# Performance work log

Measured on AMD Instinct MI355X. Metric: run time of the kernel, lower is better.

The kernel has to match this reference:

```python
import jax, jax.numpy as jnp
import numpy as np

H = 128  # hidden_size hard-coded in the torch module


def _lin(key, fan_in, shape):
    b = 1.0 / np.sqrt(fan_in)
    return jax.random.uniform(key, shape, minval=-b, maxval=b, dtype=jnp.float32)


def _gru_step(x, wih, bih, bhh):
    # torch GRU, single time step, h0 = 0; gate order (r, z, n)
    g = x @ wih.T + bih
    xr, xz, xn = jnp.split(g, 3, axis=-1)
    br, bz, bn = jnp.split(bhh, 3)
    r = jax.nn.sigmoid(xr + br)
    z = jax.nn.sigmoid(xz + bz)
    n = jnp.tanh(xn + r * bn)
    return (1.0 - z) * n  # h' = (1-z)*n + z*0


def _forward(x_node, x_edge, nt_w1, nt_b1, nt_w2, nt_b2, et_w, et_b,
             ngru_wih, ngru_bih, ngru_bhh, egru_wih, egru_bih, egru_bhh,
             natt_w, natt_b, eatt_w, eatt_b,
             lr_w1, lr_b1, lr_w2, lr_b2, cr_w1, cr_b1, cr_w2, cr_b2,
             mr_w1, mr_b1, mr_w2, mr_b2, pairs):
    B, N, _ = x_node.shape
    node_f = jax.nn.relu(x_node @ nt_w1 + nt_b1) @ nt_w2 + nt_b2      # [B,N,H]
    edge_f = x_edge @ et_w + et_b                                      # [B,N,N,H]
    nh = eh = None
    for _ in range(2):  # num_time_steps; GRU inputs are NOT updated in the original loop
        nh = _gru_step(node_f, ngru_wih, ngru_bih, ngru_bhh)           # [B,N,H]
        eh = _gru_step(edge_f, egru_wih, egru_bih, egru_bhh)           # [B,N,N,H]
        # --- node message pooling: attention over column index j ---
        n_col = jnp.broadcast_to(nh[:, :, None, :], eh.shape)          # aug[b,i,j] = nh[b,i]
        logits = (jnp.concatenate([n_col, eh], -1) @ natt_w)[..., 0] + natt_b[0]
        w = jax.nn.softmax(logits, axis=-1)                            # [B,N,N]
        nh = jnp.einsum('bijk,bij->bik', eh, w)                        # pooled node states
        # --- edge message pooling: 2-way attention over (row, col) node states ---
        n_row = jnp.broadcast_to(nh[:, None, :, :], eh.shape)          # [b,i,j] = nh[b,j]
        n_col = jnp.broadcast_to(nh[:, :, None, :], eh.shape)          # [b,i,j] = nh[b,i]
        l_row = (jnp.concatenate([n_row, eh], -1) @ eatt_w)[..., 0] + eatt_b[0]
        l_col = (jnp.concatenate([n_col, eh], -1) @ eatt_w)[..., 0] + eatt_b[0]
        w2 = jax.nn.softmax(jnp.stack([l_row, l_col], -1), axis=-1)    # [B,N,N,2]
        eh = w2[..., 0:1] * n_row + w2[..., 1:2] * n_col               # einsum('bijl,bijkl->bijk')
    # --- classifier inputs (aggregator = elementwise mean) ---
    i0, i1 = pairs[..., 0], pairs[..., 1]                              # [B,P]
    emb0 = jnp.take_along_axis(nh, i0[..., None], axis=1)              # [B,P,H]
    emb1 = jnp.take_along_axis(nh, i1[..., None], axis=1)
    bix = jnp.arange(B)[:, None]
    e01 = eh[bix, i0, i1]                                              # [B,P,H]
    e10 = eh[bix, i1, i0]
    ci = jnp.concatenate([(emb0 + emb1) * 0.5, (e01 + e10) * 0.5], -1)  # [B,P,2H]

    def head(w1, b1, wo, bo):
        return jax.nn.relu(ci @ w1 + b1) @ wo + bo

    lr = head(lr_w1, lr_b1, lr_w2, lr_b2)
    cr = head(cr_w1, cr_b1, cr_w2, cr_b2)
    mr = head(mr_w1, mr_b1, mr_w2, mr_b2)
    return jnp.concatenate([lr, cr, mr], axis=-1)                      # [B,P,6+5+3]


def setup_inputs() -> dict:
    B, N, P = 16, 64, 128
    NF, EF = 1024, 512
    CH = 512  # classifier hidden
    ks = list(jax.random.split(jax.random.key(0), 40))
    k = iter(ks)
    inp = {}
    inp['concatenated_node_features'] = jax.random.normal(next(k), (B, N, NF), dtype=jnp.float32)
    inp['interaction_feature'] = jax.random.normal(next(k), (B, N, N, EF), dtype=jnp.float32)
    inp['nt_w1'] = _lin(next(k), NF, (NF, 512)); inp['nt_b1'] = _lin(next(k), NF, (512,))
    inp['nt_w2'] = _lin(next(k), 512, (512, H)); inp['nt_b2'] = _lin(next(k), 512, (H,))
    inp['et_w'] = _lin(next(k), EF, (EF, H)); inp['et_b'] = _lin(next(k), EF, (H,))
    inp['ngru_wih'] = _lin(next(k), H, (3 * H, H))
    inp['ngru_bih'] = _lin(next(k), H, (3 * H,)); inp['ngru_bhh'] = _lin(next(k), H, (3 * H,))
    inp['egru_wih'] = _lin(next(k), H, (3 * H, H))
    inp['egru_bih'] = _lin(next(k), H, (3 * H,)); inp['egru_bhh'] = _lin(next(k), H, (3 * H,))
    inp['natt_w'] = _lin(next(k), 2 * H, (2 * H, 1)); inp['natt_b'] = _lin(next(k), 2 * H, (1,))
    inp['eatt_w'] = _lin(next(k), 2 * H, (2 * H, 1)); inp['eatt_b'] = _lin(next(k), 2 * H, (1,))
    for name, od in (('lr', 6), ('cr', 5), ('mr', 3)):
        inp[name + '_w1'] = _lin(next(k), 2 * H, (2 * H, CH))
        inp[name + '_b1'] = _lin(next(k), 2 * H, (CH,))
        inp[name + '_w2'] = _lin(next(k), CH, (CH, od))
        inp[name + '_b2'] = _lin(next(k), CH, (od,))
    inp['object_pairs'] = jax.random.randint(next(k), (B, P, 2), 0, N, dtype=jnp.int64 if jax.config.jax_enable_x64 else jnp.int32)
    inp['num_relation'] = jax.random.randint(next(k), (B,), 0, P, dtype=jnp.int64 if jax.config.jax_enable_x64 else jnp.int32)
    return inp


def reference(concatenated_node_features, interaction_feature,
              nt_w1, nt_b1, nt_w2, nt_b2, et_w, et_b,
              ngru_wih, ngru_bih, ngru_bhh, egru_wih, egru_bih, egru_bhh,
              natt_w, natt_b, eatt_w, eatt_b,
              lr_w1, lr_b1, lr_w2, lr_b2, cr_w1, cr_b1, cr_w2, cr_b2,
              mr_w1, mr_b1, mr_w2, mr_b2, object_pairs, num_relation):
    # num_relation is read but unused in the original make_classifier_inputs loop
    return _forward(concatenated_node_features, interaction_feature,
                    nt_w1, nt_b1, nt_w2, nt_b2, et_w, et_b,
                    ngru_wih, ngru_bih, ngru_bhh, egru_wih, egru_bih, egru_bhh,
                    natt_w, natt_b, eatt_w, eatt_b,
                    lr_w1, lr_b1, lr_w2, lr_b2, cr_w1, cr_b1, cr_w2, cr_b2,
                    mr_w1, mr_b1, mr_w2, mr_b2, object_pairs)
```

## Files before the change

kernel.cpp:

```cpp
#include <hip/hip_runtime.h>
#include <math.h>
#include <stdint.h>


typedef __attribute__((ext_vector_type(8))) short short8;
typedef __attribute__((ext_vector_type(4))) float f32x4;

#define DEVINL __device__ __forceinline__

DEVINL float sigmoidf_(float x) { return 1.0f / (1.0f + __expf(-x)); }
DEVINL float tanhf_(float x) {
    float e = __expf(2.0f * x);
    return (e - 1.0f) / (e + 1.0f);
}
DEVINL short bf16_rne(float f) {
    uint32_t u = __float_as_uint(f);
    u += 0x7FFFu + ((u >> 16) & 1u);
    return (short)(u >> 16);
}
DEVINL float bf16_to_f(short s) {
    return __uint_as_float(((uint32_t)(uint16_t)s) << 16);
}
DEVINL void cvt_hilo8(const float av[8], short8* h8, short8* l8) {
    union { uint32_t u[4]; short8 s; } H, L;
#pragma unroll
    for (int i = 0; i < 4; ++i) {
        float a0 = av[2 * i], a1 = av[2 * i + 1];
        uint32_t ph;
        asm("v_cvt_pk_bf16_f32 %0, %1, %2" : "=v"(ph) : "v"(a0), "v"(a1));
        float h0 = __uint_as_float(ph << 16);
        float h1 = __uint_as_float(ph & 0xFFFF0000u);
        uint32_t pl;
        asm("v_cvt_pk_bf16_f32 %0, %1, %2" : "=v"(pl) : "v"(a0 - h0), "v"(a1 - h1));
        H.u[i] = ph;
        L.u[i] = pl;
    }
    *h8 = H.s;
    *l8 = L.s;
}
DEVINL void gload_lds16(const void* g, void* l) {
    __builtin_amdgcn_global_load_lds(
        (const __attribute__((address_space(1))) void*)(uintptr_t)g,
        (__attribute__((address_space(3))) void*)(uint32_t)(uintptr_t)l,
        16, 0, 0);
}
DEVINL void ldsbar() {
    asm volatile("s_waitcnt lgkmcnt(0)\n\ts_barrier" ::: "memory");
    __builtin_amdgcn_sched_barrier(0);
}

__global__ __launch_bounds__(256) void prep_all(
    const float* __restrict__ et_w, const float* __restrict__ wih,
    const float* __restrict__ w1a, const float* __restrict__ w1b,
    const float* __restrict__ w1c,
    short* __restrict__ Bf1, short* __restrict__ Bf2,
    short* __restrict__ Wf1_hi, short* __restrict__ Wf1_lo)
{
    const int bid = blockIdx.x, t = threadIdx.x;
    if (bid < 256) {
        int idx = bid * 256 + t;
        int k = idx >> 7, n = idx & 127;
        float v = et_w[(size_t)k * 128 + n];
        short hi = bf16_rne(v);
        int kt = k >> 5, ct = n >> 4;
        int lane = (((k >> 3) & 3) << 4) | (n & 15);
        int j = k & 7;
        size_t s0 = (((size_t)kt * 8 + ct) * 64 + lane) * 8 + j;
        Bf1[s0] = hi;
    } else if (bid < 448) {
        int idx = (bid - 256) * 256 + t;
        int n = idx >> 7, k = idx & 127;
        float v = wih[(size_t)n * 128 + k];
        short hi = bf16_rne(v);
        int kt = k >> 5, ct = n >> 4;
        int lane = (((k >> 3) & 3) << 4) | (n & 15);
        int j = k & 7;
        size_t s0 = (((size_t)kt * 24 + ct) * 64 + lane) * 8 + j;
        Bf2[s0] = hi;
    } else {
        int idx = (bid - 448) * 256 + t;
        int h = idx >> 17;
        int r = idx & 131071;
        int k = r >> 9, c = r & 511;
        const float* w1 = (h == 0) ? w1a : (h == 1) ? w1b : w1c;
        float v = w1[(size_t)k * 512 + c];
        short hi = bf16_rne(v), lo = bf16_rne(v - bf16_to_f(hi));
        int kt = k >> 5, ct = c >> 4;
        int lane = (((k >> 3) & 3) << 4) | (c & 15);
        int j = k & 7;
        size_t fidx = ((((size_t)h * 8 + kt) * 32 + ct) * 64 + lane) * 8 + j;
        Wf1_hi[fidx] = hi;
        Wf1_lo[fidx] = lo;
    }
}

#define PH1_ITER(KT, BH0, BH1, NBH0, NBH1,                                    \
                 PCV0, PCV1, PLD0, PLD1, RBUF, WBUF)                          \
    {                                                                         \
        if ((KT) < 15) {                                                      \
            const short* bkt = Bf1 + (size_t)((KT) + 1) * 4096;               \
            NBH0 = *(const short8*)(bkt + ct0 * 512 + ln8);                   \
            NBH1 = *(const short8*)(bkt + ct1 * 512 + ln8);                   \
            float av[8] = {PCV0.x, PCV0.y, PCV0.z, PCV0.w,                    \
                           PCV1.x, PCV1.y, PCV1.z, PCV1.w};                   \
            short8 h8, l8;                                                    \
            cvt_hilo8(av, &h8, &l8);                                          \
            *(short8*)(smem + (WBUF) + aslotb) = h8;                          \
            *(short8*)(smem + (WBUF) + 4096 + aslotb) = l8;                   \
        }                                                                     \
        if ((KT) < 14) {                                                      \
            PLD0 = *(const float4*)(aptr + (size_t)((KT) + 2) * 32);          \
            PLD1 = *(const float4*)(aptr + (size_t)((KT) + 2) * 32 + 4);      \
        }                                                                     \
        {                                                                     \
            const char* Ah_c = smem + (RBUF);                                 \
            short8 Ahf[4], Alf[4];                                            \
            _Pragma("unroll") for (int rt = 0; rt < 4; ++rt) {                \
                Ahf[rt] = *(const short8*)(Ah_c + (rt * 64 + lane) * 16);     \
                Alf[rt] = *(const short8*)(Ah_c + 4096 + (rt * 64 + lane) * 16); \
            }                                                                 \
            _Pragma("unroll") for (int rt = 0; rt < 4; ++rt) {                \
                acc1[rt][0] = __builtin_amdgcn_mfma_f32_16x16x32_bf16(Ahf[rt], BH0, acc1[rt][0], 0, 0, 0); \
                acc1[rt][0] = __builtin_amdgcn_mfma_f32_16x16x32_bf16(Alf[rt], BH0, acc1[rt][0], 0, 0, 0); \
                acc1[rt][1] = __builtin_amdgcn_mfma_f32_16x16x32_bf16(Ahf[rt], BH1, acc1[rt][1], 0, 0, 0); \
                acc1[rt][1] = __builtin_amdgcn_mfma_f32_16x16x32_bf16(Alf[rt], BH1, acc1[rt][1], 0, 0, 0); \
            }                                                                 \
        }                                                                     \
        ldsbar();                                                             \
    }

__global__ __launch_bounds__(256, 3) void fused_kernel(
    const float* __restrict__ x_edge,
    const short* __restrict__ Bf1, const short* __restrict__ Bf2,
    const float* __restrict__ et_b,
    const float* __restrict__ bih, const float* __restrict__ bhh,
    const float* __restrict__ natt_w, const float* __restrict__ eatt_w,
    float* __restrict__ nh_p, float* __restrict__ u_out)
{
    __shared__ __align__(16) char smem[35328];
    const int t = threadIdx.x;
    const int wv = t >> 6, lane = t & 63;
    const int g = blockIdx.x;
    const size_t bm = (size_t)g * 64;

    const int arow = t >> 2, akb = t & 3;
    const int aslotb = (((arow >> 4) * 64) + ((akb << 4) | (arow & 15))) * 16;
    const float* aptr = x_edge + (bm + arow) * 512 + akb * 8;

    const int ct0 = wv * 2, ct1 = wv * 2 + 1;
    const int ln8 = lane * 8;

    f32x4 acc1[4][2] = {};

    float4 paA0, paA1, paB0, paB1;
    short8 bhA0, bhA1, bhB0, bhB1;

    paA0 = *(const float4*)(aptr);
    paA1 = *(const float4*)(aptr + 4);
    paB0 = *(const float4*)(aptr + 32);
    paB1 = *(const float4*)(aptr + 36);
    {
        const short* bkt = Bf1;
        bhA0 = *(const short8*)(bkt + ct0 * 512 + ln8);
        bhA1 = *(const short8*)(bkt + ct1 * 512 + ln8);
    }
    {
        float av[8] = {paA0.x, paA0.y, paA0.z, paA0.w,
                       paA1.x, paA1.y, paA1.z, paA1.w};
        short8 h8, l8;
        cvt_hilo8(av, &h8, &l8);
        *(short8*)(smem + aslotb) = h8;
        *(short8*)(smem + 4096 + aslotb) = l8;
    }
    ldsbar();

    for (int kt = 0; kt < 16; kt += 2) {
        PH1_ITER(kt, bhA0, bhA1, bhB0, bhB1,
                 paB0, paB1, paA0, paA1, 0, 8192)
        PH1_ITER(kt + 1, bhB0, bhB1, bhA0, bhA1,
                 paA0, paA1, paB0, paB1, 8192, 0)
    }
    __syncthreads();

    float* ef_s = (float*)smem;
#pragma unroll
    for (int c = 0; c < 2; ++c) {
        int col = wv * 32 + c * 16 + (lane & 15);
        float bias = et_b[col];
#pragma unroll
        for (int rt = 0; rt < 4; ++rt) {
#pragma unroll
            for (int q = 0; q < 4; ++q) {
                int row = rt * 16 + ((lane >> 4) << 2) + q;
                ef_s[row * 132 + col] = acc1[rt][c][q] + bias;
            }
        }
    }
    __syncthreads();

    const int EHP = 132;
    float* eh_s = (float*)smem;
#pragma unroll
    for (int rtp = 0; rtp < 2; ++rtp) {
        f32x4 acch[2][6] = {};
#pragma unroll
        for (int kt = 0; kt < 4; ++kt) {
            const short* bkt = Bf2 + (size_t)kt * 12288;
            short8 Ah[2], Al[2];
#pragma unroll
            for (int r = 0; r < 2; ++r) {
                int rt = rtp * 2 + r;
                const float* src = ef_s + (rt * 16 + (lane & 15)) * 132
                                 + kt * 32 + (lane >> 4) * 8;
                float4 v0 = *(const float4*)(src);
                float4 v1 = *(const float4*)(src + 4);
                float av[8] = {v0.x, v0.y, v0.z, v0.w, v1.x, v1.y, v1.z, v1.w};
                cvt_hilo8(av, &Ah[r], &Al[r]);
            }
#pragma unroll
            for (int c = 0; c < 6; ++c) {
                int ctg = ((c >> 1) << 3) + (wv << 1) + (c & 1);
                short8 Bh = *(const short8*)(bkt + ctg * 512 + ln8);
#pragma unroll
                for (int r = 0; r < 2; ++r) {
                    acch[r][c] = __builtin_amdgcn_mfma_f32_16x16x32_bf16(Ah[r], Bh, acch[r][c], 0, 0, 0);
                    acch[r][c] = __builtin_amdgcn_mfma_f32_16x16x32_bf16(Al[r], Bh, acch[r][c], 0, 0, 0);
                }
            }
        }
        __syncthreads();
#pragma unroll
        for (int cc = 0; cc < 2; ++cc) {
            int o = (wv << 5) + (cc << 4) + (lane & 15);
            float bco = bih[o] + bhh[o];
            float bcz = bih[128 + o] + bhh[128 + o];
            float bcn = bih[256 + o];
            float bn3 = bhh[256 + o];
#pragma unroll
            for (int r = 0; r < 2; ++r) {
#pragma unroll
                for (int q = 0; q < 4; ++q) {
                    int row = rtp * 32 + r * 16 + ((lane >> 4) << 2) + q;
                    float rr = sigmoidf_(acch[r][cc][q] + bco);
                    float zz = sigmoidf_(acch[r][2 + cc][q] + bcz);
                    float nn = tanhf_(acch[r][4 + cc][q] + bcn + rr * bn3);
                    eh_s[row * EHP + o] = (1.0f - zz) * nn;
                }
            }
        }
    }
    __syncthreads();

    float* red  = (float*)(smem + 33792);
    float* s2v  = red + 256;
    float* ewv  = s2v + 64;
    {
        int j = t >> 2, q = t & 3;
        const float* row = eh_s + j * EHP + q * 32;
        const float* wb = natt_w + 128 + q * 32;
        float a = 0.f;
#pragma unroll
        for (int k2 = 0; k2 < 32; ++k2) a = fmaf(row[k2], wb[k2], a);
        red[t] = a;
    }
    __syncthreads();
    if (t < 64) s2v[t] = red[4 * t] + red[4 * t + 1] + red[4 * t + 2] + red[4 * t + 3];
    __syncthreads();
    if (t < 64) {
        float m = -1e30f;
        for (int j = 0; j < 64; ++j) m = fmaxf(m, s2v[j]);
        ewv[t] = __expf(s2v[t] - m);
    }
    __syncthreads();
    float inv = 0.f;
    for (int j = 0; j < 64; ++j) inv += ewv[j];
    inv = 1.0f / inv;
    {
        int o = t & 127, h = t >> 7;
        float a = 0.f;
        for (int j = h * 32; j < h * 32 + 32; ++j)
            a = fmaf(ewv[j], eh_s[j * EHP + o], a);
        __syncthreads();
        red[t] = a;
    }
    __syncthreads();
    if (t < 128) {
        float v = (red[t] + red[t + 128]) * inv;
        nh_p[(size_t)g * 128 + t] = v;
        red[t] = v * eatt_w[t];
    }
    __syncthreads();
    for (int s = 64; s > 0; s >>= 1) {
        if (t < s) red[t] += red[t + s];
        __syncthreads();
    }
    if (t == 0) u_out[g] = red[0];
}

__global__ __launch_bounds__(128) void ci_kernel(
    const float* __restrict__ nh_p, const float* __restrict__ u,
    const int* __restrict__ pairs, float* __restrict__ ci)
{
    const int bp = blockIdx.x;
    const int b  = bp >> 7;
    const int t  = threadIdx.x;
    int i0 = pairs[bp * 2 + 0];
    int i1 = pairs[bp * 2 + 1];
    const float* n0 = nh_p + (size_t)(b * 64 + i0) * 128;
    const float* n1 = nh_p + (size_t)(b * 64 + i1) * 128;
    float s = sigmoidf_(u[b * 64 + i1] - u[b * 64 + i0]);
    float v0 = n0[t], v1 = n1[t];
    ci[(size_t)bp * 256 + t]       = 0.5f * (v0 + v1);
    ci[(size_t)bp * 256 + 128 + t] = s * v1 + (1.0f - s) * v0;
}

__global__ __launch_bounds__(256, 1) void headcls_kernel(
    const float* __restrict__ ci,
    const short* __restrict__ Wf1_hi, const short* __restrict__ Wf1_lo,
    const float* __restrict__ b1a, const float* __restrict__ b1b,
    const float* __restrict__ b1c,
    const float* __restrict__ w2a, const float* __restrict__ w2b,
    const float* __restrict__ w2c,
    const float* __restrict__ b2a, const float* __restrict__ b2b,
    const float* __restrict__ b2c,
    float* __restrict__ out)
{
    __shared__ __align__(16) char smem[139264];
    const int t = threadIdx.x;
    const int wv = t >> 6, lane = t & 63;
    const int rb = blockIdx.x;
    const int hd = blockIdx.y;
    const float* b1 = hd == 0 ? b1a : hd == 1 ? b1b : b1c;
    const float* w2 = hd == 0 ? w2a : hd == 1 ? w2b : w2c;
    const float* b2 = hd == 0 ? b2a : hd == 1 ? b2b : b2c;
    const int od  = hd == 0 ? 6 : hd == 1 ? 5 : 3;
    const int off = hd == 0 ? 0 : hd == 1 ? 6 : 11;

    const int arow = t >> 2, akb = t & 3;
    const int abyte = ((((arow >> 4) * 64) + ((akb << 4) | (arow & 15))) * 8) * 2;
    const float* aptr = ci + ((size_t)rb * 32 + arow) * 256 + akb * 8;

    f32x4 acc[2][8] = {};

    float4 a0, a1;
    if (t < 128) {
        a0 = *(const float4*)(aptr);
        a1 = *(const float4*)(aptr + 4);
    }
    {
        const char* sh = (const char*)(Wf1_hi + (size_t)hd * 8 * 32 * 512);
        const char* sl = (const char*)(Wf1_lo + (size_t)hd * 8 * 32 * 512);
#pragma unroll
        for (int i = 0; i < 8; ++i) {
            int ch = i * 4 + wv;
            int o2 = ch * 1024 + lane * 16;
            gload_lds16(sh + o2, smem + ch * 1024);
            gload_lds16(sl + o2, smem + 32768 + ch * 1024);
        }
    }
    if (t < 128) {
        float av[8] = {a0.x, a0.y, a0.z, a0.w, a1.x, a1.y, a1.z, a1.w};
        short8 h8, l8;
        cvt_hilo8(av, &h8, &l8);
        *(short8*)(smem + 131072 + abyte) = h8;
        *(short8*)(smem + 131072 + 2048 + abyte) = l8;
    }
    __syncthreads();

    for (int kt = 0; kt < 8; ++kt) {
        const int cur = kt & 1;
        const char* Bh_c = smem + cur * 65536;
        const char* Bl_c = Bh_c + 32768;
        const char* Ah_c = smem + 131072 + cur * 4096;
        const char* Al_c = Ah_c + 2048;

        float4 b0, b1v;
        if (kt < 7) {
            const char* sh = (const char*)(Wf1_hi + ((size_t)hd * 8 + kt + 1) * 32 * 512);
            const char* sl = (const char*)(Wf1_lo + ((size_t)hd * 8 + kt + 1) * 32 * 512);
            char* dBh = smem + (cur ^ 1) * 65536;
#pragma unroll
            for (int i = 0; i < 8; ++i) {
                int ch = i * 4 + wv;
                int o2 = ch * 1024 + lane * 16;
                gload_lds16(sh + o2, dBh + ch * 1024);
                gload_lds16(sl + o2, dBh + 32768 + ch * 1024);
            }
            if (t < 128) {
                b0  = *(const float4*)(aptr + (size_t)(kt + 1) * 32);
                b1v = *(const float4*)(aptr + (size_t)(kt + 1) * 32 + 4);
            }
        }

        short8 Ah[2], Al[2];
#pragma unroll
        for (int rt = 0; rt < 2; ++rt) {
            Ah[rt] = *(const short8*)(Ah_c + (rt * 64 + lane) * 16);
            Al[rt] = *(const short8*)(Al_c + (rt * 64 + lane) * 16);
        }
#pragma unroll
        for (int c = 0; c < 8; ++c) {
            int ctg = wv * 8 + c;
            short8 Bh = *(const short8*)(Bh_c + (ctg * 64 + lane) * 16);
            short8 Bl = *(const short8*)(Bl_c + (ctg * 64 + lane) * 16);
#pragma unroll
            for (int rt = 0; rt < 2; ++rt) {
                acc[rt][c] = __builtin_amdgcn_mfma_f32_16x16x32_bf16(Ah[rt], Bh, acc[rt][c], 0, 0, 0);
                acc[rt][c] = __builtin_amdgcn_mfma_f32_16x16x32_bf16(Al[rt], Bh, acc[rt][c], 0, 0, 0);
                acc[rt][c] = __builtin_amdgcn_mfma_f32_16x16x32_bf16(Ah[rt], Bl, acc[rt][c], 0, 0, 0);
            }
        }

        if (kt < 7 && t < 128) {
            float av[8] = {b0.x, b0.y, b0.z, b0.w, b1v.x, b1v.y, b1v.z, b1v.w};
            short8 h8, l8;
            cvt_hilo8(av, &h8, &l8);
            char* dAh = smem + 131072 + (cur ^ 1) * 4096;
            *(short8*)(dAh + abyte) = h8;
            *(short8*)(dAh + 2048 + abyte) = l8;
        }
        __syncthreads();
    }

    float* h_s  = (float*)smem;
    float* w2_s = (float*)(smem + 66048);
    for (int idx = t; idx < 512 * od; idx += 256) w2_s[idx] = w2[idx];
#pragma unroll
    for (int c = 0; c < 8; ++c) {
        int ctg = wv * 8 + c;
        int col = ctg * 16 + (lane & 15);
        float bias = b1[col];
#pragma unroll
        for (int rt = 0; rt < 2; ++rt) {
#pragma unroll
            for (int q = 0; q < 4; ++q) {
                int row = rt * 16 + ((lane >> 4) << 2) + q;
                h_s[row * 516 + col] = fmaxf(acc[rt][c][q] + bias, 0.f);
            }
        }
    }
    __syncthreads();

    {
        int row = t >> 3, o = t & 7;
        if (o < od) {
            const float* hr = h_s + row * 516;
            float a = b2[o];
            for (int c = 0; c < 512; ++c)
                a = fmaf(hr[c], w2_s[c * od + o], a);
            out[((size_t)rb * 32 + row) * 14 + off + o] = a;
        }
    }
}

extern "C" void kernel_launch(void* const* d_in, const int* in_sizes, int n_in,
                              void* d_out, int out_size, void* d_ws, size_t ws_size,
                              hipStream_t stream)
{
    const float* x_edge   = (const float*)d_in[1];
    const float* et_w     = (const float*)d_in[6];
    const float* et_b     = (const float*)d_in[7];
    const float* egru_wih = (const float*)d_in[11];
    const float* egru_bih = (const float*)d_in[12];
    const float* egru_bhh = (const float*)d_in[13];
    const float* natt_w   = (const float*)d_in[14];
    const float* eatt_w   = (const float*)d_in[16];
    const float* lr_w1 = (const float*)d_in[18];
    const float* lr_b1 = (const float*)d_in[19];
    const float* lr_w2 = (const float*)d_in[20];
    const float* lr_b2 = (const float*)d_in[21];
    const float* cr_w1 = (const float*)d_in[22];
    const float* cr_b1 = (const float*)d_in[23];
    const float* cr_w2 = (const float*)d_in[24];
    const float* cr_b2 = (const float*)d_in[25];
    const float* mr_w1 = (const float*)d_in[26];
    const float* mr_b1 = (const float*)d_in[27];
    const float* mr_w2 = (const float*)d_in[28];
    const float* mr_b2 = (const float*)d_in[29];
    const int* pairs   = (const int*)d_in[30];
    float* out = (float*)d_out;
    char* ws = (char*)d_ws;

    short* Bf1    = (short*)(ws + 0);
    short* Bf2    = (short*)(ws + 131072);
    short* Wf1_hi = (short*)(ws + 229376);
    short* Wf1_lo = (short*)(ws + 1015808);
    float* nh_p   = (float*)(ws + 1802240);
    float* u      = (float*)(ws + 2326528);
    float* ci     = (float*)(ws + 2330624);

    prep_all<<<1984, 256, 0, stream>>>(et_w, egru_wih, lr_w1, cr_w1, mr_w1,
                                       Bf1, Bf2, Wf1_hi, Wf1_lo);

    fused_kernel<<<1024, 256, 0, stream>>>(
        x_edge, Bf1, Bf2, et_b, egru_bih, egru_bhh, natt_w, eatt_w, nh_p, u);

    ci_kernel<<<2048, 128, 0, stream>>>(nh_p, u, pairs, ci);

    headcls_kernel<<<dim3(64, 3), 256, 0, stream>>>(
        ci, Wf1_hi, Wf1_lo, lr_b1, cr_b1, mr_b1,
        lr_w2, cr_w2, mr_w2, lr_b2, cr_b2, mr_b2, out);
}
```

Measured before the change: 83.30 us.

## Process two 64-row groups per 512-thread block to share B-fragment loads

Each block now handles 128 rows of edge features with 512 threads (8 waves), split into two row-quarters that share the same column tiles. The staging buffers double in size, and the later attention and pooling stages run independently per 64-row half using separate reduction scratch. The aim is to halve the grid size and let waves in a block reuse the same weight fragments, which cuts per-block overhead. In exchange, LDS use per block doubles and block-wide barriers now stall twice as many waves.

```diff
diff --git a/kernel.cpp b/kernel.cpp
--- a/kernel.cpp
+++ b/kernel.cpp
@@ -106,7 +106,7 @@
             short8 h8, l8;                                                    \
             cvt_hilo8(av, &h8, &l8);                                          \
             *(short8*)(smem + (WBUF) + aslotb) = h8;                          \
-            *(short8*)(smem + (WBUF) + 4096 + aslotb) = l8;                   \
+            *(short8*)(smem + (WBUF) + 8192 + aslotb) = l8;                   \
         }                                                                     \
         if ((KT) < 14) {                                                      \
             PLD0 = *(const float4*)(aptr + (size_t)((KT) + 2) * 32);          \
@@ -116,8 +116,9 @@
             const char* Ah_c = smem + (RBUF);                                 \
             short8 Ahf[4], Alf[4];                                            \
             _Pragma("unroll") for (int rt = 0; rt < 4; ++rt) {                \
-                Ahf[rt] = *(const short8*)(Ah_c + (rt * 64 + lane) * 16);     \
-                Alf[rt] = *(const short8*)(Ah_c + 4096 + (rt * 64 + lane) * 16); \
+                int grt = rq * 4 + rt;                                        \
+                Ahf[rt] = *(const short8*)(Ah_c + (grt * 64 + lane) * 16);    \
+                Alf[rt] = *(const short8*)(Ah_c + 8192 + (grt * 64 + lane) * 16); \
             }                                                                 \
             _Pragma("unroll") for (int rt = 0; rt < 4; ++rt) {                \
                 acc1[rt][0] = __builtin_amdgcn_mfma_f32_16x16x32_bf16(Ahf[rt], BH0, acc1[rt][0], 0, 0, 0); \
@@ -129,7 +130,7 @@
         ldsbar();                                                             \
     }
 
-__global__ __launch_bounds__(256, 3) void fused_kernel(
+__global__ __launch_bounds__(512, 2) void fused_kernel(
     const float* __restrict__ x_edge,
     const short* __restrict__ Bf1, const short* __restrict__ Bf2,
     const float* __restrict__ et_b,
@@ -137,17 +138,18 @@
     const float* __restrict__ natt_w, const float* __restrict__ eatt_w,
     float* __restrict__ nh_p, float* __restrict__ u_out)
 {
-    __shared__ __align__(16) char smem[35328];
+    __shared__ __align__(16) char smem[70656];
     const int t = threadIdx.x;
     const int wv = t >> 6, lane = t & 63;
-    const int g = blockIdx.x;
-    const size_t bm = (size_t)g * 64;
+    const int cq = wv & 3, rq = wv >> 2;
+    const int g2 = blockIdx.x;
+    const size_t bm = (size_t)g2 * 128;
 
     const int arow = t >> 2, akb = t & 3;
     const int aslotb = (((arow >> 4) * 64) + ((akb << 4) | (arow & 15))) * 16;
     const float* aptr = x_edge + (bm + arow) * 512 + akb * 8;
 
-    const int ct0 = wv * 2, ct1 = wv * 2 + 1;
+    const int ct0 = cq * 2, ct1 = cq * 2 + 1;
     const int ln8 = lane * 8;
 
     f32x4 acc1[4][2] = {};
@@ -170,28 +172,28 @@
         short8 h8, l8;
         cvt_hilo8(av, &h8, &l8);
         *(short8*)(smem + aslotb) = h8;
-        *(short8*)(smem + 4096 + aslotb) = l8;
+        *(short8*)(smem + 8192 + aslotb) = l8;
     }
     ldsbar();
 
     for (int kt = 0; kt < 16; kt += 2) {
         PH1_ITER(kt, bhA0, bhA1, bhB0, bhB1,
-                 paB0, paB1, paA0, paA1, 0, 8192)
+                 paB0, paB1, paA0, paA1, 0, 16384)
         PH1_ITER(kt + 1, bhB0, bhB1, bhA0, bhA1,
-                 paA0, paA1, paB0, paB1, 8192, 0)
+                 paA0, paA1, paB0, paB1, 16384, 0)
     }
     __syncthreads();
 
     float* ef_s = (float*)smem;
 #pragma unroll
     for (int c = 0; c < 2; ++c) {
-        int col = wv * 32 + c * 16 + (lane & 15);
+        int col = cq * 32 + c * 16 + (lane & 15);
         float bias = et_b[col];
 #pragma unroll
         for (int rt = 0; rt < 4; ++rt) {
 #pragma unroll
             for (int q = 0; q < 4; ++q) {
-                int row = rt * 16 + ((lane >> 4) << 2) + q;
+                int row = rq * 64 + rt * 16 + ((lane >> 4) << 2) + q;
                 ef_s[row * 132 + col] = acc1[rt][c][q] + bias;
             }
         }
@@ -199,7 +201,7 @@
     __syncthreads();
 
     const int EHP = 132;
-    float* eh_s = (float*)smem;
+    float* ef_t = (float*)smem + rq * (64 * EHP);
 #pragma unroll
     for (int rtp = 0; rtp < 2; ++rtp) {
         f32x4 acch[2][6] = {};
@@ -210,7 +212,7 @@
 #pragma unroll
             for (int r = 0; r < 2; ++r) {
                 int rt = rtp * 2 + r;
-                const float* src = ef_s + (rt * 16 + (lane & 15)) * 132
+                const float* src = ef_t + (rt * 16 + (lane & 15)) * 132
                                  + kt * 32 + (lane >> 4) * 8;
                 float4 v0 = *(const float4*)(src);
                 float4 v1 = *(const float4*)(src + 4);
@@ -219,7 +221,7 @@
             }
 #pragma unroll
             for (int c = 0; c < 6; ++c) {
-                int ctg = ((c >> 1) << 3) + (wv << 1) + (c & 1);
+                int ctg = ((c >> 1) << 3) + (cq << 1) + (c & 1);
                 short8 Bh = *(const short8*)(bkt + ctg * 512 + ln8);
 #pragma unroll
                 for (int r = 0; r < 2; ++r) {
@@ -231,7 +233,7 @@
         __syncthreads();
 #pragma unroll
         for (int cc = 0; cc < 2; ++cc) {
-            int o = (wv << 5) + (cc << 4) + (lane & 15);
+            int o = (cq << 5) + (cc << 4) + (lane & 15);
             float bco = bih[o] + bhh[o];
             float bcz = bih[128 + o] + bhh[128 + o];
             float bcn = bih[256 + o];
@@ -244,57 +246,60 @@
                     float rr = sigmoidf_(acch[r][cc][q] + bco);
                     float zz = sigmoidf_(acch[r][2 + cc][q] + bcz);
                     float nn = tanhf_(acch[r][4 + cc][q] + bcn + rr * bn3);
-                    eh_s[row * EHP + o] = (1.0f - zz) * nn;
+                    ef_t[row * EHP + o] = (1.0f - zz) * nn;
                 }
             }
         }
     }
     __syncthreads();
 
-    float* red  = (float*)(smem + 33792);
+    const int tt = cq * 64 + lane;
+    const int G = g2 * 2 + rq;
+    float* eh_g = ef_t;
+    float* red  = (float*)(smem + 67584 + rq * 1536);
     float* s2v  = red + 256;
     float* ewv  = s2v + 64;
     {
-        int j = t >> 2, q = t & 3;
-        const float* row = eh_s + j * EHP + q * 32;
+        int j = tt >> 2, q = tt & 3;
+        const float* row = eh_g + j * EHP + q * 32;
         const float* wb = natt_w + 128 + q * 32;
         float a = 0.f;
 #pragma unroll
         for (int k2 = 0; k2 < 32; ++k2) a = fmaf(row[k2], wb[k2], a);
-        red[t] = a;
-    }
-    __syncthreads();
-    if (t < 64) s2v[t] = red[4 * t] + red[4 * t + 1] + red[4 * t + 2] + red[4 * t + 3];
-    __syncthreads();
-    if (t < 64) {
+        red[tt] = a;
+    }
+    __syncthreads();
+    if (tt < 64) s2v[tt] = red[4 * tt] + red[4 * tt + 1] + red[4 * tt + 2] + red[4 * tt + 3];
+    __syncthreads();
+    if (tt < 64) {
         float m = -1e30f;
         for (int j = 0; j < 64; ++j) m = fmaxf(m, s2v[j]);
-        ewv[t] = __expf(s2v[t] - m);
+        ewv[tt] = __expf(s2v[tt] - m);
     }
     __syncthreads();
     float inv = 0.f;
     for (int j = 0; j < 64; ++j) inv += ewv[j];
     inv = 1.0f / inv;
     {
-        int o = t & 127, h = t >> 7;
+        int o = tt & 127, h = tt >> 7;
         float a = 0.f;
         for (int j = h * 32; j < h * 32 + 32; ++j)
-            a = fmaf(ewv[j], eh_s[j * EHP + o], a);
+            a = fmaf(ewv[j], eh_g[j * EHP + o], a);
         __syncthreads();
-        red[t] = a;
-    }
-    __syncthreads();
-    if (t < 128) {
-        float v = (red[t] + red[t + 128]) * inv;
-        nh_p[(size_t)g * 128 + t] = v;
-        red[t] = v * eatt_w[t];
+        red[tt] = a;
+    }
+    __syncthreads();
+    if (tt < 128) {
+        float v = (red[tt] + red[tt + 128]) * inv;
+        nh_p[(size_t)G * 128 + tt] = v;
+        red[tt] = v * eatt_w[tt];
     }
     __syncthreads();
     for (int s = 64; s > 0; s >>= 1) {
-        if (t < s) red[t] += red[t + s];
+        if (tt < s) red[tt] += red[tt + s];
         __syncthreads();
     }
-    if (t == 0) u_out[g] = red[0];
+    if (tt == 0) u_out[G] = red[0];
 }
 
 __global__ __launch_bounds__(128) void ci_kernel(
@@ -492,7 +497,7 @@
     prep_all<<<1984, 256, 0, stream>>>(et_w, egru_wih, lr_w1, cr_w1, mr_w1,
                                        Bf1, Bf2, Wf1_hi, Wf1_lo);
 
-    fused_kernel<<<1024, 256, 0, stream>>>(
+    fused_kernel<<<512, 512, 0, stream>>>(
         x_edge, Bf1, Bf2, et_b, egru_bih, egru_bhh, natt_w, eatt_w, nh_p, u);
 
     ci_kernel<<<2048, 128, 0, stream>>>(nh_p, u, pairs, ci);
```

New measurement: 100.6 us. +20.7%, slower.
